# Kernel optimization log

Hardware: AMD Instinct MI355X
Metric: run time of the kernel (lower is better)

## Reference

```python
import jax, jax.numpy as jnp
import numpy as np

D_MODEL, NHEAD = 256, 8
HEAD_DIM = D_MODEL // NHEAD  # 32, also the conv group count


def layer_norm(x, w, b, eps=1e-5):
    mu = jnp.mean(x, axis=-1, keepdims=True)
    var = jnp.var(x, axis=-1, keepdims=True)
    return (x - mu) * jax.lax.rsqrt(var + eps) * w + b


def setup_inputs() -> dict:
    key = jax.random.key(0)
    ks = jax.random.split(key, 12)
    b, H, W = 4, 120, 160
    L = H * W  # 19200; 'self' path requires L == H*W
    d, h = D_MODEL, NHEAD
    s = 0.05
    p = lambda i, shape: jax.random.normal(ks[i], shape, jnp.float32) * s
    return {
        "x": jax.random.normal(ks[0], (b, L, d), jnp.float32),
        "source": jax.random.normal(ks[1], (b, L, d), jnp.float32),
        "Wq": p(2, (d, d)), "Wk": p(3, (d, d)), "Wv": p(4, (d, d)),
        "Wmerge": p(5, (d, d)),
        "Wmlp1": p(6, (2 * d, 2 * d)), "Wmlp2": p(7, (2 * d, d)),
        "ln1_w": jnp.ones((d,), jnp.float32), "ln1_b": jnp.zeros((d,), jnp.float32),
        "ln2_w": jnp.ones((d,), jnp.float32), "ln2_b": jnp.zeros((d,), jnp.float32),
        "Wdown": p(8, (2 * d, 64)), "Wup": p(9, (64, d)),
        "fc_w": p(10, (9, 3 * h)), "fc_b": jnp.zeros((9,), jnp.float32),
        "dep_w": p(11, (d, 9, 3, 3)),  # torch OIHW layout, groups=32 (O/g=8, I/g=9)
        "dep_b": jnp.zeros((d,), jnp.float32),
        "rate": jnp.full((1,), 0.5, jnp.float32),
        "H": H, "W": W,
    }


def reference(x, source, Wq, Wk, Wv, Wmerge, Wmlp1, Wmlp2,
              ln1_w, ln1_b, ln2_w, ln2_b, Wdown, Wup,
              fc_w, fc_b, dep_w, dep_b, rate, H, W):
    # name == 'self' path is hardcoded (conv branch active)
    b, L, d = x.shape
    h, hd = NHEAD, HEAD_DIM
    S = source.shape[1]

    q = (x @ Wq).reshape(b, L, h, hd)
    k = (source @ Wk).reshape(b, S, h, hd)
    v = (source @ Wv).reshape(b, S, h, hd)

    # ---- conv branch ----
    # [b, L, h, 3*hd] -> [b, L, 3h, hd] -> [b, 3h, L, hd]
    f_all = jnp.concatenate([q, k, v], axis=-1).reshape(b, L, 3 * h, hd)
    f_all = jnp.transpose(f_all, (0, 2, 1, 3))
    # 1x1 conv 3h -> 9 over (L, hd) 'spatial' grid
    f9 = jnp.einsum('oc,bcld->bold', fc_w, f_all) + fc_b[None, :, None, None]
    # [b, 9, L, hd] -> [b, hd, 9, L] -> [b, 9*hd, H, W]
    f_conv = jnp.transpose(f9, (0, 3, 1, 2)).reshape(b, 9 * hd, H, W)
    out_conv = jax.lax.conv_general_dilated(
        f_conv, dep_w, window_strides=(1, 1), padding=((1, 1), (1, 1)),
        feature_group_count=hd, dimension_numbers=('NCHW', 'OIHW', 'NCHW'))
    out_conv = out_conv + dep_b[None, :, None, None]
    out_conv = jnp.transpose(out_conv, (0, 2, 3, 1)).reshape(b, L, d)

    # ---- linear attention (elu+1 feature map), O(N) ----
    Qf = jax.nn.elu(q) + 1.0
    Kf = jax.nn.elu(k) + 1.0
    v_len = jnp.float32(S)
    vals = v / v_len
    KV = jnp.einsum('bshd,bshv->bhdv', Kf, vals)
    Z = 1.0 / (jnp.einsum('blhd,bhd->blh', Qf, Kf.sum(axis=1)) + 1e-6)
    message = jnp.einsum('blhd,bhdv,blh->blhv', Qf, KV, Z) * v_len

    # ---- merge / norm / MLP / adapter ----
    message = message.reshape(b, L, d) @ Wmerge
    message = layer_norm(message, ln1_w, ln1_b)
    cat1 = jnp.concatenate([x, message], axis=2)
    message = jax.nn.relu(cat1 @ Wmlp1) @ Wmlp2
    message = layer_norm(message, ln2_w, ln2_b)

    cat2 = jnp.concatenate([x, message], axis=2)
    up = jax.nn.relu(cat2 @ Wdown) @ Wup
    message = message + up * 0.1
    message = message + rate * out_conv
    return x + message
```

## Files before the change

kernel.cpp:

```cpp
#include <hip/hip_runtime.h>
#include <stdint.h>

#define LL 19200
#define NBATCH 4
#define NROWS (NBATCH * LL)
#define HH 120
#define WW 160

typedef short bhalf8 __attribute__((ext_vector_type(8)));
typedef float f32x4 __attribute__((ext_vector_type(4)));

__device__ __forceinline__ float bfbits2f(uint32_t u) { union { uint32_t i; float f; } c; c.i = u << 16; return c.f; }
__device__ __forceinline__ float bf2f(uint16_t h) { return bfbits2f((uint32_t)h); }
__device__ __forceinline__ uint16_t f2bf(float f) {
    union { float f; uint32_t i; } c; c.f = f;
    return (uint16_t)((c.i + 0x7FFFu + ((c.i >> 16) & 1u)) >> 16);
}
__device__ __forceinline__ uint32_t pk2(uint16_t a, uint16_t b) { return (uint32_t)a | ((uint32_t)b << 16); }
__device__ __forceinline__ float elup1(float x) { return x > 0.f ? x + 1.f : expf(x); }

__device__ __forceinline__ uint4 pack8f(const float* p) {
    float4 lo = *(const float4*)p; float4 hi = *(const float4*)(p + 4);
    uint4 s;
    s.x = pk2(f2bf(lo.x), f2bf(lo.y)); s.y = pk2(f2bf(lo.z), f2bf(lo.w));
    s.z = pk2(f2bf(hi.x), f2bf(hi.y)); s.w = pk2(f2bf(hi.z), f2bf(hi.w));
    return s;
}

__device__ __forceinline__ void gll16(const void* g, void* l) {
    __builtin_amdgcn_global_load_lds((const __attribute__((address_space(1))) uint32_t*)g,
                                     (__attribute__((address_space(3))) uint32_t*)l, 16, 0, 0);
}

__global__ __launch_bounds__(256) void prep_wt(const float* __restrict__ src, uint16_t* __restrict__ dst,
                                               int K, int Nout) {
    int idx = blockIdx.x * 256 + threadIdx.x;
    if (idx >= K * Nout) return;
    int n = idx / K, kk = idx - n * K;
    dst[idx] = f2bf(src[(long)kk * Nout + n]);
}

#define EPI_NONE 0
#define EPI_RELU 1
#define EPI_LN 2
#define EPI_FINAL 3

template<int BN, int MODE_A, int EPI>
__global__ __launch_bounds__(512)
void gemm_big(const float* __restrict__ A0f, const uint16_t* __restrict__ A0b,
              const uint16_t* __restrict__ A1b,
              const uint16_t* __restrict__ Wt, int K,
              uint16_t* __restrict__ outb, float* __restrict__ outf, int outW,
              const float* __restrict__ lnw, const float* __restrict__ lnb,
              const float* __restrict__ xres, const uint16_t* __restrict__ msg2res,
              const uint16_t* __restrict__ convres, const float* __restrict__ ratep)
{
    constexpr int WCOLS = BN / 64;
    constexpr int WROWS = 8 / WCOLS;
    constexpr int MT = 128 / (WROWS * 16);
    __shared__ __align__(16) uint16_t a_sm[128 * 32];
    __shared__ __align__(16) uint16_t b_sm[BN * 32];
    const int tid = threadIdx.x;
    const int lane = tid & 63;
    const int wv = tid >> 6;
    const int wr = wv / WCOLS, wc = wv % WCOLS;
    const long row0 = (long)blockIdx.x * 128;
    const int col0 = blockIdx.y * BN;

    f32x4 acc[MT][4];
#pragma unroll
    for (int m = 0; m < MT; ++m)
#pragma unroll
        for (int n = 0; n < 4; ++n) acc[m][n] = (f32x4){0.f, 0.f, 0.f, 0.f};

    const int sr = tid >> 2;
    const int sc = (tid & 3) * 8;
    const long argA = row0 + sr;
    uint16_t* a_dst = a_sm + (tid >> 6) * 512;
    uint16_t* b_dst = b_sm + (tid >> 6) * 512;

    for (int k0 = 0; k0 < K; k0 += 32) {
        if (MODE_A == 0) {
            gll16(A0b + argA * (long)K + k0 + sc, a_dst);
        } else if (MODE_A == 1) {
            *(uint4*)&a_sm[sr * 32 + sc] = pack8f(A0f + argA * (long)K + k0 + sc);
        } else {
            if (k0 < 256) *(uint4*)&a_sm[sr * 32 + sc] = pack8f(A0f + argA * 256 + k0 + sc);
            else          gll16(A1b + argA * 256 + (k0 - 256) + sc, a_dst);
        }
        if (BN == 256) {
            gll16(Wt + (long)(col0 + sr) * K + k0 + sc, b_dst);
            gll16(Wt + (long)(col0 + 128 + sr) * K + k0 + sc, b_sm + 4096 + (tid >> 6) * 512);
        } else {
            if (tid < 256) gll16(Wt + (long)(col0 + sr) * K + k0 + sc, b_dst);
        }
        __syncthreads();
        bhalf8 af[MT];
#pragma unroll
        for (int m = 0; m < MT; ++m)
            af[m] = *(const bhalf8*)&a_sm[(wr * MT * 16 + m * 16 + (lane & 15)) * 32 + (lane >> 4) * 8];
#pragma unroll
        for (int n = 0; n < 4; ++n) {
            bhalf8 bfr = *(const bhalf8*)&b_sm[(wc * 64 + n * 16 + (lane & 15)) * 32 + (lane >> 4) * 8];
#pragma unroll
            for (int m = 0; m < MT; ++m)
                acc[m][n] = __builtin_amdgcn_mfma_f32_16x16x32_bf16(af[m], bfr, acc[m][n], 0, 0, 0);
        }
        __syncthreads();
    }

    const int cl = lane & 15;
    const int rg4 = (lane >> 4) * 4;

    if constexpr (EPI == EPI_LN) {
        __shared__ float red_s[4][128];
        __shared__ float red_ss[4][128];
#pragma unroll
        for (int m = 0; m < MT; ++m)
#pragma unroll
            for (int j = 0; j < 4; ++j) {
                float p = 0.f, pp = 0.f;
#pragma unroll
                for (int n = 0; n < 4; ++n) { float v = acc[m][n][j]; p += v; pp += v * v; }
#pragma unroll
                for (int msk = 1; msk < 16; msk <<= 1) { p += __shfl_xor(p, msk, 64); pp += __shfl_xor(pp, msk, 64); }
                if (cl == 0) {
                    int lr = wr * 64 + m * 16 + rg4 + j;
                    red_s[wc][lr] = p; red_ss[wc][lr] = pp;
                }
            }
        __syncthreads();
#pragma unroll
        for (int m = 0; m < MT; ++m)
#pragma unroll
            for (int j = 0; j < 4; ++j) {
                int lr = wr * 64 + m * 16 + rg4 + j;
                float s = red_s[0][lr] + red_s[1][lr] + red_s[2][lr] + red_s[3][lr];
                float ss = red_ss[0][lr] + red_ss[1][lr] + red_ss[2][lr] + red_ss[3][lr];
                float mu = s * (1.f / 256.f);
                float var = ss * (1.f / 256.f) - mu * mu;
                float rstd = rsqrtf(var + 1e-5f);
                long rowg = row0 + lr;
#pragma unroll
                for (int n = 0; n < 4; ++n) {
                    int col = wc * 64 + n * 16 + cl;
                    float vv = (acc[m][n][j] - mu) * rstd * lnw[col] + lnb[col];
                    outb[rowg * (long)outW + col] = f2bf(vv);
                }
            }
    } else if constexpr (EPI == EPI_FINAL) {
        float rate = ratep[0];
#pragma unroll
        for (int m = 0; m < MT; ++m)
#pragma unroll
            for (int j = 0; j < 4; ++j) {
                long rowg = row0 + wr * MT * 16 + m * 16 + rg4 + j;
                int bb = (int)(rowg / LL);
                int ll = (int)(rowg - (long)bb * LL);
#pragma unroll
                for (int n = 0; n < 4; ++n) {
                    int col = wc * 64 + n * 16 + cl;
                    long o = rowg * 256 + col;
                    float xv = xres[o];
                    float m2 = bf2f(msg2res[o]);
                    float cv = bf2f(convres[((long)(bb * 256 + col)) * LL + ll]);
                    outf[o] = xv + m2 + 0.1f * acc[m][n][j] + rate * cv;
                }
            }
    } else {
#pragma unroll
        for (int m = 0; m < MT; ++m)
#pragma unroll
            for (int j = 0; j < 4; ++j) {
                long rowg = row0 + wr * MT * 16 + m * 16 + rg4 + j;
#pragma unroll
                for (int n = 0; n < 4; ++n) {
                    int col = col0 + wc * 64 + n * 16 + cl;
                    float vv = acc[m][n][j];
                    if (EPI == EPI_RELU) vv = vv > 0.f ? vv : 0.f;
                    outb[rowg * (long)outW + col] = f2bf(vv);
                }
            }
    }
}

__global__ __launch_bounds__(256)
void kv_partial(const uint16_t* __restrict__ kb, const uint16_t* __restrict__ vb,
                float* __restrict__ part) {
    __shared__ float kf_sm[32][33];
    __shared__ float v_sm[32][33];
    const int tid = threadIdx.x;
    const int bh = blockIdx.y, b = bh >> 3, h = bh & 7;
    const int s0 = blockIdx.x * 256;
    const int d = tid >> 3, vg = tid & 7;
    const int sl = tid >> 3, e4 = (tid & 7) * 4;
    float a0 = 0.f, a1 = 0.f, a2 = 0.f, a3 = 0.f, aKs = 0.f;
    for (int it = 0; it < 8; ++it) {
        long base = ((long)(b * LL + s0 + it * 32 + sl)) * 256 + h * 32 + e4;
        uint2 kk = *(const uint2*)(kb + base);
        uint2 vv = *(const uint2*)(vb + base);
        kf_sm[sl][e4 + 0] = elup1(bfbits2f(kk.x & 0xFFFFu));
        kf_sm[sl][e4 + 1] = elup1(bfbits2f(kk.x >> 16));
        kf_sm[sl][e4 + 2] = elup1(bfbits2f(kk.y & 0xFFFFu));
        kf_sm[sl][e4 + 3] = elup1(bfbits2f(kk.y >> 16));
        v_sm[sl][e4 + 0] = bfbits2f(vv.x & 0xFFFFu);
        v_sm[sl][e4 + 1] = bfbits2f(vv.x >> 16);
        v_sm[sl][e4 + 2] = bfbits2f(vv.y & 0xFFFFu);
        v_sm[sl][e4 + 3] = bfbits2f(vv.y >> 16);
        __syncthreads();
#pragma unroll 8
        for (int s = 0; s < 32; ++s) {
            float kf = kf_sm[s][d];
            aKs += kf;
            const float* vp = &v_sm[s][vg * 4];
            a0 += kf * vp[0]; a1 += kf * vp[1]; a2 += kf * vp[2]; a3 += kf * vp[3];
        }
        __syncthreads();
    }
    long pb = ((long)(blockIdx.x * 32 + bh)) * 1056;
    part[pb + d * 32 + vg * 4 + 0] = a0;
    part[pb + d * 32 + vg * 4 + 1] = a1;
    part[pb + d * 32 + vg * 4 + 2] = a2;
    part[pb + d * 32 + vg * 4 + 3] = a3;
    if (vg == 0) part[pb + 1024 + d] = aKs;
}

__global__ __launch_bounds__(256)
void kv_final(const float* __restrict__ part, float* __restrict__ KVg, float* __restrict__ Ksum) {
    const int bh = blockIdx.x, tid = threadIdx.x;
    for (int idx = tid; idx < 1056; idx += 256) {
        float s = 0.f;
        for (int c = 0; c < 75; ++c) s += part[((long)(c * 32 + bh)) * 1056 + idx];
        if (idx < 1024) KVg[bh * 1024 + idx] = s;
        else Ksum[bh * 32 + idx - 1024] = s;
    }
}

__global__ __launch_bounds__(256)
void attn_msg(const uint16_t* __restrict__ qb, const float* __restrict__ KVg,
              const float* __restrict__ Ksum, uint16_t* __restrict__ msgout) {
    __shared__ float kv_sm[8192];
    __shared__ float ks_sm[256];
    __shared__ float qf_sm[8][264];
    const int tid = threadIdx.x;
    const int b = blockIdx.y;
    const long l0 = (long)blockIdx.x * 64;
    for (int idx = tid; idx < 8192; idx += 256) kv_sm[idx] = KVg[b * 8192 + idx];
    ks_sm[tid] = Ksum[b * 256 + tid];
    __syncthreads();
    const int h = tid >> 5, vc = tid & 31;
    const int rr = tid >> 5, e8 = (tid & 31) * 8;
    for (int r0 = 0; r0 < 64; r0 += 8) {
        long rowg = (long)b * LL + l0 + r0 + rr;
        uint4 qv = *(const uint4*)(qb + rowg * 256 + e8);
        qf_sm[rr][e8 + 0] = elup1(bfbits2f(qv.x & 0xFFFFu));
        qf_sm[rr][e8 + 1] = elup1(bfbits2f(qv.x >> 16));
        qf_sm[rr][e8 + 2] = elup1(bfbits2f(qv.y & 0xFFFFu));
        qf_sm[rr][e8 + 3] = elup1(bfbits2f(qv.y >> 16));
        qf_sm[rr][e8 + 4] = elup1(bfbits2f(qv.z & 0xFFFFu));
        qf_sm[rr][e8 + 5] = elup1(bfbits2f(qv.z >> 16));
        qf_sm[rr][e8 + 6] = elup1(bfbits2f(qv.w & 0xFFFFu));
        qf_sm[rr][e8 + 7] = elup1(bfbits2f(qv.w >> 16));
        __syncthreads();
        for (int r2 = 0; r2 < 8; ++r2) {
            float p = qf_sm[r2][h * 32 + vc] * ks_sm[h * 32 + vc];
#pragma unroll
            for (int m = 1; m < 32; m <<= 1) p += __shfl_xor(p, m, 64);
            float Z = 1.f / (p + 1e-6f);
            float acc = 0.f;
#pragma unroll
            for (int dd = 0; dd < 32; ++dd)
                acc += qf_sm[r2][h * 32 + dd] * kv_sm[(h * 32 + dd) * 32 + vc];
            long orow = (long)b * LL + l0 + r0 + r2;
            msgout[orow * 256 + tid] = f2bf(acc * Z);
        }
        __syncthreads();
    }
}

__global__ __launch_bounds__(256)
void f9_kernel(const uint16_t* __restrict__ qb, const uint16_t* __restrict__ kb,
               const uint16_t* __restrict__ vb, const float* __restrict__ fcw,
               const float* __restrict__ fcb, uint16_t* __restrict__ fconv) {
    __shared__ __align__(16) uint16_t sm[3][32][264];
    __shared__ float fw[9][24];
    __shared__ float fb[9];
    const int tid = threadIdx.x;
    const int b = blockIdx.y;
    const int l0 = blockIdx.x * 32;
    if (tid < 216) fw[tid / 24][tid % 24] = fcw[tid];
    if (tid >= 216 && tid < 225) fb[tid - 216] = fcb[tid - 216];
    for (int idx = tid; idx < 3072; idx += 256) {
        int tsr = idx >> 10, rem = idx & 1023, row = rem >> 5, c8 = (rem & 31) * 8;
        const uint16_t* src = tsr == 0 ? qb : (tsr == 1 ? kb : vb);
        *(uint4*)&sm[tsr][row][c8] = *(const uint4*)(src + ((long)(b * LL + l0 + row)) * 256 + c8);
    }
    __syncthreads();
    for (int idx = tid; idx < 9216; idx += 256) {
        int ch = idx >> 5, li = idx & 31;
        int dp = ch / 9, o = ch - dp * 9;
        float acc = fb[o];
#pragma unroll
        for (int hd = 0; hd < 8; ++hd) {
            int cb = hd * 32 + dp;
            acc += fw[o][3 * hd + 0] * bf2f(sm[0][li][cb]);
            acc += fw[o][3 * hd + 1] * bf2f(sm[1][li][cb]);
            acc += fw[o][3 * hd + 2] * bf2f(sm[2][li][cb]);
        }
        fconv[((long)(b * 288 + ch)) * LL + l0 + li] = f2bf(acc);
    }
}

__global__ __launch_bounds__(256)
void dwconv2(const uint16_t* __restrict__ fconv, const float* __restrict__ depw,
             const float* __restrict__ depb, uint16_t* __restrict__ convout) {
    __shared__ __align__(16) uint16_t in_sm[9][26][48];
    __shared__ float w_sm[8][81];
    __shared__ float b_sm2[8];
    const int tid = threadIdx.x;
    const int bg = blockIdx.z, b = bg >> 5, g = bg & 31;
    const int y0 = blockIdx.y * 24;
    const int x0 = blockIdx.x * 32;
    for (int idx = tid; idx < 648; idx += 256)
        w_sm[idx / 81][idx % 81] = depw[(long)(g * 8) * 81 + idx];
    if (tid < 8) b_sm2[tid] = depb[g * 8 + tid];
    for (int rIdx = tid; rIdx < 234; rIdx += 256) {
        int i = rIdx / 26, r = rIdx - i * 26;
        int yy = y0 + r - 1;
        uint16_t* dst = &in_sm[i][r][0];
        if (yy >= 0 && yy < HH) {
            const uint16_t* rp = fconv + ((long)(b * 288 + g * 9 + i)) * LL + yy * WW;
            *(uint4*)&dst[8]  = *(const uint4*)(rp + x0);
            *(uint4*)&dst[16] = *(const uint4*)(rp + x0 + 8);
            *(uint4*)&dst[24] = *(const uint4*)(rp + x0 + 16);
            *(uint4*)&dst[32] = *(const uint4*)(rp + x0 + 24);
            dst[7]  = (x0 > 0) ? rp[x0 - 1] : (uint16_t)0;
            dst[40] = (x0 + 32 < WW) ? rp[x0 + 32] : (uint16_t)0;
        } else {
            uint4 z = {0, 0, 0, 0};
            *(uint4*)&dst[8] = z; *(uint4*)&dst[16] = z;
            *(uint4*)&dst[24] = z; *(uint4*)&dst[32] = z;
            dst[7] = 0; dst[40] = 0;
        }
    }
    __syncthreads();
    const int xc = tid & 7, m = (tid >> 3) & 7, ys = tid >> 6;
    float acc[6][4];
    float bias = b_sm2[m];
#pragma unroll
    for (int r = 0; r < 6; ++r)
#pragma unroll
        for (int o = 0; o < 4; ++o) acc[r][o] = bias;
    for (int i = 0; i < 9; ++i) {
        float w[9];
#pragma unroll
        for (int t = 0; t < 9; ++t) w[t] = w_sm[m][i * 9 + t];
#pragma unroll
        for (int rr = 0; rr < 8; ++rr) {
            const uint16_t* rowb = &in_sm[i][ys * 6 + rr][4 + xc * 4];
            uint2 lo = *(const uint2*)rowb;
            uint2 hi = *(const uint2*)(rowb + 4);
            uint32_t ex = *(const uint32_t*)(rowb + 8);
            float f[6];
            f[0] = bfbits2f(lo.y >> 16);
            f[1] = bfbits2f(hi.x & 0xFFFFu);
            f[2] = bfbits2f(hi.x >> 16);
            f[3] = bfbits2f(hi.y & 0xFFFFu);
            f[4] = bfbits2f(hi.y >> 16);
            f[5] = bfbits2f(ex & 0xFFFFu);
#pragma unroll
            for (int ky = 0; ky < 3; ++ky) {
                int ro = rr - ky;
                if (ro >= 0 && ro < 6) {
#pragma unroll
                    for (int o = 0; o < 4; ++o)
                        acc[ro][o] += w[ky * 3 + 0] * f[o] + w[ky * 3 + 1] * f[o + 1] + w[ky * 3 + 2] * f[o + 2];
                }
            }
        }
    }
    long chbase = ((long)(b * 256 + g * 8 + m)) * LL;
#pragma unroll
    for (int rl = 0; rl < 6; ++rl) {
        int y = y0 + ys * 6 + rl;
        uint2 st;
        st.x = pk2(f2bf(acc[rl][0]), f2bf(acc[rl][1]));
        st.y = pk2(f2bf(acc[rl][2]), f2bf(acc[rl][3]));
        *(uint2*)(convout + chbase + (long)y * WW + x0 + xc * 4) = st;
    }
}

extern "C" void kernel_launch(void* const* d_in, const int* in_sizes, int n_in,
                              void* d_out, int out_size, void* d_ws, size_t ws_size,
                              hipStream_t stream) {
    (void)in_sizes; (void)n_in; (void)out_size; (void)ws_size;
    const float* x      = (const float*)d_in[0];
    const float* src    = (const float*)d_in[1];
    const float* Wq     = (const float*)d_in[2];
    const float* Wk     = (const float*)d_in[3];
    const float* Wv     = (const float*)d_in[4];
    const float* Wmerge = (const float*)d_in[5];
    const float* Wmlp1  = (const float*)d_in[6];
    const float* Wmlp2  = (const float*)d_in[7];
    const float* ln1w   = (const float*)d_in[8];
    const float* ln1b   = (const float*)d_in[9];
    const float* ln2w   = (const float*)d_in[10];
    const float* ln2b   = (const float*)d_in[11];
    const float* Wdown  = (const float*)d_in[12];
    const float* Wup    = (const float*)d_in[13];
    const float* fcw    = (const float*)d_in[14];
    const float* fcb    = (const float*)d_in[15];
    const float* depw   = (const float*)d_in[16];
    const float* depb   = (const float*)d_in[17];
    const float* rate   = (const float*)d_in[18];

    char* ws = (char*)d_ws;
    const size_t SZ_NB = (size_t)NROWS * 256 * 2;
    const size_t O_Q = 0;
    const size_t O_K = SZ_NB;
    const size_t O_V = 2 * SZ_NB;
    const size_t O_FCONV = 3 * SZ_NB;
    const size_t O_CONVOUT = O_FCONV + (size_t)NBATCH * 288 * LL * 2;
    const size_t O_PART = O_CONVOUT + SZ_NB;
    const size_t O_KV = O_PART + (size_t)75 * 32 * 1056 * 4;
    const size_t O_KS = O_KV + (size_t)32 * 1024 * 4;
    const size_t O_WT = O_KS + (size_t)32 * 32 * 4;

    uint16_t* qB      = (uint16_t*)(ws + O_Q);
    uint16_t* kB      = (uint16_t*)(ws + O_K);
    uint16_t* vB      = (uint16_t*)(ws + O_V);
    uint16_t* fconv   = (uint16_t*)(ws + O_FCONV);
    uint16_t* convout = (uint16_t*)(ws + O_CONVOUT);
    float*    part    = (float*)(ws + O_PART);
    float*    KVg     = (float*)(ws + O_KV);
    float*    Ksg     = (float*)(ws + O_KS);
    uint16_t* wt_q    = (uint16_t*)(ws + O_WT);
    uint16_t* wt_k    = wt_q + 256 * 256;
    uint16_t* wt_v    = wt_k + 256 * 256;
    uint16_t* wt_m    = wt_v + 256 * 256;
    uint16_t* wt_m1   = wt_m + 256 * 256;
    uint16_t* wt_m2   = wt_m1 + 512 * 512;
    uint16_t* wt_d    = wt_m2 + 512 * 256;
    uint16_t* wt_u    = wt_d + 512 * 64;
    uint16_t* msgattn = kB;
    uint16_t* msgB    = vB;
    uint16_t* hidden  = qB;
    uint16_t* msg2    = fconv;
    uint16_t* h2      = (uint16_t*)(ws + O_PART);

    prep_wt<<<256, 256, 0, stream>>>(Wq, wt_q, 256, 256);
    prep_wt<<<256, 256, 0, stream>>>(Wk, wt_k, 256, 256);
    prep_wt<<<256, 256, 0, stream>>>(Wv, wt_v, 256, 256);
    prep_wt<<<256, 256, 0, stream>>>(Wmerge, wt_m, 256, 256);
    prep_wt<<<1024, 256, 0, stream>>>(Wmlp1, wt_m1, 512, 512);
    prep_wt<<<512, 256, 0, stream>>>(Wmlp2, wt_m2, 512, 256);
    prep_wt<<<128, 256, 0, stream>>>(Wdown, wt_d, 512, 64);
    prep_wt<<<64, 256, 0, stream>>>(Wup, wt_u, 64, 256);

    const dim3 g600(NROWS / 128, 1);
    gemm_big<256, 1, EPI_NONE><<<g600, 512, 0, stream>>>(x, nullptr, nullptr, wt_q, 256, qB, nullptr, 256,
        nullptr, nullptr, nullptr, nullptr, nullptr, nullptr);
    gemm_big<256, 1, EPI_NONE><<<g600, 512, 0, stream>>>(src, nullptr, nullptr, wt_k, 256, kB, nullptr, 256,
        nullptr, nullptr, nullptr, nullptr, nullptr, nullptr);
    gemm_big<256, 1, EPI_NONE><<<g600, 512, 0, stream>>>(src, nullptr, nullptr, wt_v, 256, vB, nullptr, 256,
        nullptr, nullptr, nullptr, nullptr, nullptr, nullptr);
    kv_partial<<<dim3(75, 32), 256, 0, stream>>>(kB, vB, part);
    kv_final<<<32, 256, 0, stream>>>(part, KVg, Ksg);
    f9_kernel<<<dim3(LL / 32, NBATCH), 256, 0, stream>>>(qB, kB, vB, fcw, fcb, fconv);
    dwconv2<<<dim3(5, 5, 128), 256, 0, stream>>>(fconv, depw, depb, convout);
    attn_msg<<<dim3(LL / 64, NBATCH), 256, 0, stream>>>(qB, KVg, Ksg, msgattn);
    gemm_big<256, 0, EPI_LN><<<g600, 512, 0, stream>>>(nullptr, msgattn, nullptr, wt_m, 256, msgB, nullptr, 256,
        ln1w, ln1b, nullptr, nullptr, nullptr, nullptr);
    gemm_big<256, 2, EPI_RELU><<<dim3(NROWS / 128, 2), 512, 0, stream>>>(x, nullptr, msgB, wt_m1, 512, hidden, nullptr, 512,
        nullptr, nullptr, nullptr, nullptr, nullptr, nullptr);
    gemm_big<256, 0, EPI_LN><<<g600, 512, 0, stream>>>(nullptr, hidden, nullptr, wt_m2, 512, msg2, nullptr, 256,
        ln2w, ln2b, nullptr, nullptr, nullptr, nullptr);
    gemm_big<64, 2, EPI_RELU><<<g600, 512, 0, stream>>>(x, nullptr, msg2, wt_d, 512, h2, nullptr, 64,
        nullptr, nullptr, nullptr, nullptr, nullptr, nullptr);
    gemm_big<256, 0, EPI_FINAL><<<g600, 512, 0, stream>>>(nullptr, h2, nullptr, wt_u, 64, nullptr, (float*)d_out, 256,
        nullptr, nullptr, x, msg2, convout, rate);
}
```

Baseline: 956.8 us.

## Cache bf16 copies of inputs, MFMA attention, swizzled f9, fused weight prep

Several independent changes land together. The Q and K projections now write bf16 copies of x and source as a side output, and later GEMMs (V, MLP1, down-projection and the final residual) read these instead of reloading and repacking fp32, which cuts input bandwidth. The attention-message kernel is rewritten around MFMA 16x16x32 bf16 tiles, f9_kernel is restructured with XOR-swizzled LDS and register accumulation, kv_partial uses float4 LDS accesses, and the eight weight-prep launches become one. Reading x as bf16 for the final residual adds rounding error to the output, and the bf16-copy path only runs when the workspace is large enough.

```diff
diff --git a/kernel.cpp b/kernel.cpp
--- a/kernel.cpp
+++ b/kernel.cpp
@@ -32,12 +32,29 @@
                                      (__attribute__((address_space(3))) uint32_t*)l, 16, 0, 0);
 }
 
-__global__ __launch_bounds__(256) void prep_wt(const float* __restrict__ src, uint16_t* __restrict__ dst,
-                                               int K, int Nout) {
-    int idx = blockIdx.x * 256 + threadIdx.x;
-    if (idx >= K * Nout) return;
+__global__ __launch_bounds__(256)
+void prep_all(const float* __restrict__ Wq, const float* __restrict__ Wk,
+              const float* __restrict__ Wv, const float* __restrict__ Wm,
+              const float* __restrict__ Wm1, const float* __restrict__ Wm2,
+              const float* __restrict__ Wd, const float* __restrict__ Wu,
+              uint16_t* __restrict__ wq, uint16_t* __restrict__ wk,
+              uint16_t* __restrict__ wvv, uint16_t* __restrict__ wm,
+              uint16_t* __restrict__ wm1, uint16_t* __restrict__ wm2,
+              uint16_t* __restrict__ wd, uint16_t* __restrict__ wu) {
+    int blk = blockIdx.x;
+    const float* s; uint16_t* d; int K, N, base;
+    if (blk < 1024) {
+        int which = blk >> 8; base = which << 8;
+        s = which == 0 ? Wq : which == 1 ? Wk : which == 2 ? Wv : Wm;
+        d = which == 0 ? wq : which == 1 ? wk : which == 2 ? wvv : wm;
+        K = 256; N = 256;
+    } else if (blk < 2048) { s = Wm1; d = wm1; K = 512; N = 512; base = 1024; }
+    else if (blk < 2560)   { s = Wm2; d = wm2; K = 512; N = 256; base = 2048; }
+    else if (blk < 2688)   { s = Wd;  d = wd;  K = 512; N = 64;  base = 2560; }
+    else                   { s = Wu;  d = wu;  K = 64;  N = 256; base = 2688; }
+    int idx = (blk - base) * 256 + threadIdx.x;
     int n = idx / K, kk = idx - n * K;
-    dst[idx] = f2bf(src[(long)kk * Nout + n]);
+    d[idx] = f2bf(s[(long)kk * N + n]);
 }
 
 #define EPI_NONE 0
@@ -51,8 +68,10 @@
               const uint16_t* __restrict__ A1b,
               const uint16_t* __restrict__ Wt, int K,
               uint16_t* __restrict__ outb, float* __restrict__ outf, int outW,
+              uint16_t* __restrict__ sideout,
               const float* __restrict__ lnw, const float* __restrict__ lnb,
-              const float* __restrict__ xres, const uint16_t* __restrict__ msg2res,
+              const float* __restrict__ xres, const uint16_t* __restrict__ xresb,
+              const uint16_t* __restrict__ msg2res,
               const uint16_t* __restrict__ convres, const float* __restrict__ ratep)
 {
     constexpr int WCOLS = BN / 64;
@@ -76,21 +95,27 @@
     const int sr = tid >> 2;
     const int sc = (tid & 3) * 8;
     const long argA = row0 + sr;
-    uint16_t* a_dst = a_sm + (tid >> 6) * 512;
-    uint16_t* b_dst = b_sm + (tid >> 6) * 512;
+    uint16_t* a_dst = a_sm + wv * 512;
+    uint16_t* b_dst = b_sm + wv * 512;
 
     for (int k0 = 0; k0 < K; k0 += 32) {
         if (MODE_A == 0) {
             gll16(A0b + argA * (long)K + k0 + sc, a_dst);
         } else if (MODE_A == 1) {
-            *(uint4*)&a_sm[sr * 32 + sc] = pack8f(A0f + argA * (long)K + k0 + sc);
-        } else {
+            uint4 stg = pack8f(A0f + argA * (long)K + k0 + sc);
+            *(uint4*)&a_sm[sr * 32 + sc] = stg;
+            if (sideout) *(uint4*)(sideout + argA * (long)K + k0 + sc) = stg;
+        } else if (MODE_A == 2) {
             if (k0 < 256) *(uint4*)&a_sm[sr * 32 + sc] = pack8f(A0f + argA * 256 + k0 + sc);
             else          gll16(A1b + argA * 256 + (k0 - 256) + sc, a_dst);
+        } else {
+            const uint16_t* srcp = (k0 < 256) ? (A0b + argA * 256 + k0 + sc)
+                                              : (A1b + argA * 256 + (k0 - 256) + sc);
+            gll16(srcp, a_dst);
         }
         if (BN == 256) {
             gll16(Wt + (long)(col0 + sr) * K + k0 + sc, b_dst);
-            gll16(Wt + (long)(col0 + 128 + sr) * K + k0 + sc, b_sm + 4096 + (tid >> 6) * 512);
+            gll16(Wt + (long)(col0 + 128 + sr) * K + k0 + sc, b_sm + 4096 + wv * 512);
         } else {
             if (tid < 256) gll16(Wt + (long)(col0 + sr) * K + k0 + sc, b_dst);
         }
@@ -161,7 +186,7 @@
                 for (int n = 0; n < 4; ++n) {
                     int col = wc * 64 + n * 16 + cl;
                     long o = rowg * 256 + col;
-                    float xv = xres[o];
+                    float xv = xresb ? bf2f(xresb[o]) : xres[o];
                     float m2 = bf2f(msg2res[o]);
                     float cv = bf2f(convres[((long)(bb * 256 + col)) * LL + ll]);
                     outf[o] = xv + m2 + 0.1f * acc[m][n][j] + rate * cv;
@@ -188,7 +213,7 @@
 void kv_partial(const uint16_t* __restrict__ kb, const uint16_t* __restrict__ vb,
                 float* __restrict__ part) {
     __shared__ float kf_sm[32][33];
-    __shared__ float v_sm[32][33];
+    __shared__ float v_sm[32][36];
     const int tid = threadIdx.x;
     const int bh = blockIdx.y, b = bh >> 3, h = bh & 7;
     const int s0 = blockIdx.x * 256;
@@ -203,17 +228,17 @@
         kf_sm[sl][e4 + 1] = elup1(bfbits2f(kk.x >> 16));
         kf_sm[sl][e4 + 2] = elup1(bfbits2f(kk.y & 0xFFFFu));
         kf_sm[sl][e4 + 3] = elup1(bfbits2f(kk.y >> 16));
-        v_sm[sl][e4 + 0] = bfbits2f(vv.x & 0xFFFFu);
-        v_sm[sl][e4 + 1] = bfbits2f(vv.x >> 16);
-        v_sm[sl][e4 + 2] = bfbits2f(vv.y & 0xFFFFu);
-        v_sm[sl][e4 + 3] = bfbits2f(vv.y >> 16);
+        float4 vf;
+        vf.x = bfbits2f(vv.x & 0xFFFFu); vf.y = bfbits2f(vv.x >> 16);
+        vf.z = bfbits2f(vv.y & 0xFFFFu); vf.w = bfbits2f(vv.y >> 16);
+        *(float4*)&v_sm[sl][e4] = vf;
         __syncthreads();
 #pragma unroll 8
         for (int s = 0; s < 32; ++s) {
             float kf = kf_sm[s][d];
             aKs += kf;
-            const float* vp = &v_sm[s][vg * 4];
-            a0 += kf * vp[0]; a1 += kf * vp[1]; a2 += kf * vp[2]; a3 += kf * vp[3];
+            float4 v4 = *(const float4*)&v_sm[s][vg * 4];
+            a0 += kf * v4.x; a1 += kf * v4.y; a2 += kf * v4.z; a3 += kf * v4.w;
         }
         __syncthreads();
     }
@@ -237,44 +262,57 @@
 }
 
 __global__ __launch_bounds__(256)
-void attn_msg(const uint16_t* __restrict__ qb, const float* __restrict__ KVg,
-              const float* __restrict__ Ksum, uint16_t* __restrict__ msgout) {
-    __shared__ float kv_sm[8192];
-    __shared__ float ks_sm[256];
-    __shared__ float qf_sm[8][264];
+void attn_mfma(const uint16_t* __restrict__ qb, const float* __restrict__ KVg,
+               const float* __restrict__ Ksum, uint16_t* __restrict__ msgout) {
     const int tid = threadIdx.x;
-    const int b = blockIdx.y;
+    const int lane = tid & 63;
+    const int wv = tid >> 6;
     const long l0 = (long)blockIdx.x * 64;
-    for (int idx = tid; idx < 8192; idx += 256) kv_sm[idx] = KVg[b * 8192 + idx];
-    ks_sm[tid] = Ksum[b * 256 + tid];
-    __syncthreads();
-    const int h = tid >> 5, vc = tid & 31;
-    const int rr = tid >> 5, e8 = (tid & 31) * 8;
-    for (int r0 = 0; r0 < 64; r0 += 8) {
-        long rowg = (long)b * LL + l0 + r0 + rr;
-        uint4 qv = *(const uint4*)(qb + rowg * 256 + e8);
-        qf_sm[rr][e8 + 0] = elup1(bfbits2f(qv.x & 0xFFFFu));
-        qf_sm[rr][e8 + 1] = elup1(bfbits2f(qv.x >> 16));
-        qf_sm[rr][e8 + 2] = elup1(bfbits2f(qv.y & 0xFFFFu));
-        qf_sm[rr][e8 + 3] = elup1(bfbits2f(qv.y >> 16));
-        qf_sm[rr][e8 + 4] = elup1(bfbits2f(qv.z & 0xFFFFu));
-        qf_sm[rr][e8 + 5] = elup1(bfbits2f(qv.z >> 16));
-        qf_sm[rr][e8 + 6] = elup1(bfbits2f(qv.w & 0xFFFFu));
-        qf_sm[rr][e8 + 7] = elup1(bfbits2f(qv.w >> 16));
-        __syncthreads();
-        for (int r2 = 0; r2 < 8; ++r2) {
-            float p = qf_sm[r2][h * 32 + vc] * ks_sm[h * 32 + vc];
-#pragma unroll
-            for (int m = 1; m < 32; m <<= 1) p += __shfl_xor(p, m, 64);
-            float Z = 1.f / (p + 1e-6f);
-            float acc = 0.f;
-#pragma unroll
-            for (int dd = 0; dd < 32; ++dd)
-                acc += qf_sm[r2][h * 32 + dd] * kv_sm[(h * 32 + dd) * 32 + vc];
-            long orow = (long)b * LL + l0 + r0 + r2;
-            msgout[orow * 256 + tid] = f2bf(acc * Z);
-        }
-        __syncthreads();
+    const int b = (int)(l0 / LL);
+    const int l15 = lane & 15, lk = lane >> 4;
+#pragma unroll
+    for (int hi = 0; hi < 2; ++hi) {
+        const int h = wv * 2 + hi;
+        const float* kvb = KVg + ((long)(b * 8 + h)) * 1024;
+        const float* ksb = Ksum + (b * 8 + h) * 32;
+        bhalf8 B0, B1;
+        float ks[8];
+#pragma unroll
+        for (int i = 0; i < 8; ++i) {
+            int k = lk * 8 + i;
+            B0[i] = (short)f2bf(kvb[k * 32 + l15]);
+            B1[i] = (short)f2bf(kvb[k * 32 + 16 + l15]);
+            ks[i] = ksb[k];
+        }
+#pragma unroll
+        for (int rt = 0; rt < 4; ++rt) {
+            long row = l0 + rt * 16 + l15;
+            uint4 qv = *(const uint4*)(qb + row * 256 + h * 32 + lk * 8);
+            float qf[8];
+            qf[0] = elup1(bfbits2f(qv.x & 0xFFFFu)); qf[1] = elup1(bfbits2f(qv.x >> 16));
+            qf[2] = elup1(bfbits2f(qv.y & 0xFFFFu)); qf[3] = elup1(bfbits2f(qv.y >> 16));
+            qf[4] = elup1(bfbits2f(qv.z & 0xFFFFu)); qf[5] = elup1(bfbits2f(qv.z >> 16));
+            qf[6] = elup1(bfbits2f(qv.w & 0xFFFFu)); qf[7] = elup1(bfbits2f(qv.w >> 16));
+            bhalf8 A;
+#pragma unroll
+            for (int i = 0; i < 8; ++i) A[i] = (short)f2bf(qf[i]);
+            float p = qf[0]*ks[0] + qf[1]*ks[1] + qf[2]*ks[2] + qf[3]*ks[3]
+                    + qf[4]*ks[4] + qf[5]*ks[5] + qf[6]*ks[6] + qf[7]*ks[7];
+            p += __shfl_xor(p, 16, 64);
+            p += __shfl_xor(p, 32, 64);
+            f32x4 d0 = (f32x4){0.f,0.f,0.f,0.f}, d1 = (f32x4){0.f,0.f,0.f,0.f};
+            d0 = __builtin_amdgcn_mfma_f32_16x16x32_bf16(A, B0, d0, 0, 0, 0);
+            d1 = __builtin_amdgcn_mfma_f32_16x16x32_bf16(A, B1, d1, 0, 0, 0);
+#pragma unroll
+            for (int j = 0; j < 4; ++j) {
+                int orl = lk * 4 + j;
+                float zr = __shfl(p, orl, 64);
+                float Z = 1.f / (zr + 1e-6f);
+                long orow = l0 + rt * 16 + orl;
+                msgout[orow * 256 + h * 32 + l15]      = f2bf(d0[j] * Z);
+                msgout[orow * 256 + h * 32 + 16 + l15] = f2bf(d1[j] * Z);
+            }
+        }
     }
 }
 
@@ -282,32 +320,55 @@
 void f9_kernel(const uint16_t* __restrict__ qb, const uint16_t* __restrict__ kb,
                const uint16_t* __restrict__ vb, const float* __restrict__ fcw,
                const float* __restrict__ fcb, uint16_t* __restrict__ fconv) {
-    __shared__ __align__(16) uint16_t sm[3][32][264];
-    __shared__ float fw[9][24];
-    __shared__ float fb[9];
+    __shared__ __align__(16) uint16_t sm[3 * 32 * 256];
+    char* smb = (char*)sm;
     const int tid = threadIdx.x;
     const int b = blockIdx.y;
     const int l0 = blockIdx.x * 32;
-    if (tid < 216) fw[tid / 24][tid % 24] = fcw[tid];
-    if (tid >= 216 && tid < 225) fb[tid - 216] = fcb[tid - 216];
     for (int idx = tid; idx < 3072; idx += 256) {
-        int tsr = idx >> 10, rem = idx & 1023, row = rem >> 5, c8 = (rem & 31) * 8;
+        int tsr = idx >> 10, row = (idx >> 5) & 31, c = idx & 31;
         const uint16_t* src = tsr == 0 ? qb : (tsr == 1 ? kb : vb);
-        *(uint4*)&sm[tsr][row][c8] = *(const uint4*)(src + ((long)(b * LL + l0 + row)) * 256 + c8);
+        uint4 v = *(const uint4*)(src + ((long)(b * LL + l0 + row)) * 256 + c * 8);
+        int boff = (c * 16) ^ ((row & 7) << 4);
+        *(uint4*)(smb + (tsr * 32 + row) * 512 + boff) = v;
     }
     __syncthreads();
-    for (int idx = tid; idx < 9216; idx += 256) {
-        int ch = idx >> 5, li = idx & 31;
-        int dp = ch / 9, o = ch - dp * 9;
-        float acc = fb[o];
-#pragma unroll
-        for (int hd = 0; hd < 8; ++hd) {
-            int cb = hd * 32 + dp;
-            acc += fw[o][3 * hd + 0] * bf2f(sm[0][li][cb]);
-            acc += fw[o][3 * hd + 1] * bf2f(sm[1][li][cb]);
-            acc += fw[o][3 * hd + 2] * bf2f(sm[2][li][cb]);
-        }
-        fconv[((long)(b * 288 + ch)) * LL + l0 + li] = f2bf(acc);
+    const int li = tid & 31, g = tid >> 5;
+    float acc[9][4];
+#pragma unroll
+    for (int o = 0; o < 9; ++o) {
+        float bv = fcb[o];
+#pragma unroll
+        for (int j = 0; j < 4; ++j) acc[o][j] = bv;
+    }
+    const int swz = (li & 7) << 4;
+#pragma unroll
+    for (int h = 0; h < 8; ++h) {
+        float f[3][4];
+#pragma unroll
+        for (int s = 0; s < 3; ++s) {
+            int boff = (h * 64 + g * 8) ^ swz;
+            uint2 r = *(const uint2*)(smb + (s * 32 + li) * 512 + boff);
+            f[s][0] = bfbits2f(r.x & 0xFFFFu); f[s][1] = bfbits2f(r.x >> 16);
+            f[s][2] = bfbits2f(r.y & 0xFFFFu); f[s][3] = bfbits2f(r.y >> 16);
+        }
+#pragma unroll
+        for (int o = 0; o < 9; ++o) {
+            float w0 = fcw[o * 24 + 3 * h + 0];
+            float w1 = fcw[o * 24 + 3 * h + 1];
+            float w2 = fcw[o * 24 + 3 * h + 2];
+#pragma unroll
+            for (int j = 0; j < 4; ++j)
+                acc[o][j] += w0 * f[0][j] + w1 * f[1][j] + w2 * f[2][j];
+        }
+    }
+    const long ob = (long)(b * 288) * LL + l0 + li;
+#pragma unroll
+    for (int j = 0; j < 4; ++j) {
+        int dp = g * 4 + j;
+#pragma unroll
+        for (int o = 0; o < 9; ++o)
+            fconv[ob + (long)(dp * 9 + o) * LL] = f2bf(acc[o][j]);
     }
 }
 
@@ -344,7 +405,7 @@
         }
     }
     __syncthreads();
-    const int xc = tid & 7, m = (tid >> 3) & 7, ys = tid >> 6;
+    const int xi = tid & 7, m = (tid >> 3) & 7, ys = tid >> 6;
     float acc[6][4];
     float bias = b_sm2[m];
 #pragma unroll
@@ -357,7 +418,7 @@
         for (int t = 0; t < 9; ++t) w[t] = w_sm[m][i * 9 + t];
 #pragma unroll
         for (int rr = 0; rr < 8; ++rr) {
-            const uint16_t* rowb = &in_sm[i][ys * 6 + rr][4 + xc * 4];
+            const uint16_t* rowb = &in_sm[i][ys * 6 + rr][4 + xi * 4];
             uint2 lo = *(const uint2*)rowb;
             uint2 hi = *(const uint2*)(rowb + 4);
             uint32_t ex = *(const uint32_t*)(rowb + 8);
@@ -386,14 +447,14 @@
         uint2 st;
         st.x = pk2(f2bf(acc[rl][0]), f2bf(acc[rl][1]));
         st.y = pk2(f2bf(acc[rl][2]), f2bf(acc[rl][3]));
-        *(uint2*)(convout + chbase + (long)y * WW + x0 + xc * 4) = st;
+        *(uint2*)(convout + chbase + (long)y * WW + x0 + xi * 4) = st;
     }
 }
 
 extern "C" void kernel_launch(void* const* d_in, const int* in_sizes, int n_in,
                               void* d_out, int out_size, void* d_ws, size_t ws_size,
                               hipStream_t stream) {
-    (void)in_sizes; (void)n_in; (void)out_size; (void)ws_size;
+    (void)in_sizes; (void)n_in; (void)out_size;
     const float* x      = (const float*)d_in[0];
     const float* src    = (const float*)d_in[1];
     const float* Wq     = (const float*)d_in[2];
@@ -425,6 +486,9 @@
     const size_t O_KV = O_PART + (size_t)75 * 32 * 1056 * 4;
     const size_t O_KS = O_KV + (size_t)32 * 1024 * 4;
     const size_t O_WT = O_KS + (size_t)32 * 32 * 4;
+    const size_t O_XB = O_WT + 704512 * 2 + 1024;
+    const size_t O_SRCB = O_XB + SZ_NB;
+    const size_t NEED = O_SRCB + SZ_NB;
 
     uint16_t* qB      = (uint16_t*)(ws + O_Q);
     uint16_t* kB      = (uint16_t*)(ws + O_K);
@@ -442,41 +506,54 @@
     uint16_t* wt_m2   = wt_m1 + 512 * 512;
     uint16_t* wt_d    = wt_m2 + 512 * 256;
     uint16_t* wt_u    = wt_d + 512 * 64;
+    uint16_t* xb      = (uint16_t*)(ws + O_XB);
+    uint16_t* srcb    = (uint16_t*)(ws + O_SRCB);
     uint16_t* msgattn = kB;
     uint16_t* msgB    = vB;
     uint16_t* hidden  = qB;
     uint16_t* msg2    = fconv;
     uint16_t* h2      = (uint16_t*)(ws + O_PART);
 
-    prep_wt<<<256, 256, 0, stream>>>(Wq, wt_q, 256, 256);
-    prep_wt<<<256, 256, 0, stream>>>(Wk, wt_k, 256, 256);
-    prep_wt<<<256, 256, 0, stream>>>(Wv, wt_v, 256, 256);
-    prep_wt<<<256, 256, 0, stream>>>(Wmerge, wt_m, 256, 256);
-    prep_wt<<<1024, 256, 0, stream>>>(Wmlp1, wt_m1, 512, 512);
-    prep_wt<<<512, 256, 0, stream>>>(Wmlp2, wt_m2, 512, 256);
-    prep_wt<<<128, 256, 0, stream>>>(Wdown, wt_d, 512, 64);
-    prep_wt<<<64, 256, 0, stream>>>(Wup, wt_u, 64, 256);
+    const bool big = ws_size >= NEED;
+
+    prep_all<<<2752, 256, 0, stream>>>(Wq, Wk, Wv, Wmerge, Wmlp1, Wmlp2, Wdown, Wup,
+                                       wt_q, wt_k, wt_v, wt_m, wt_m1, wt_m2, wt_d, wt_u);
 
     const dim3 g600(NROWS / 128, 1);
     gemm_big<256, 1, EPI_NONE><<<g600, 512, 0, stream>>>(x, nullptr, nullptr, wt_q, 256, qB, nullptr, 256,
-        nullptr, nullptr, nullptr, nullptr, nullptr, nullptr);
+        big ? xb : nullptr, nullptr, nullptr, nullptr, nullptr, nullptr, nullptr, nullptr);
     gemm_big<256, 1, EPI_NONE><<<g600, 512, 0, stream>>>(src, nullptr, nullptr, wt_k, 256, kB, nullptr, 256,
-        nullptr, nullptr, nullptr, nullptr, nullptr, nullptr);
-    gemm_big<256, 1, EPI_NONE><<<g600, 512, 0, stream>>>(src, nullptr, nullptr, wt_v, 256, vB, nullptr, 256,
-        nullptr, nullptr, nullptr, nullptr, nullptr, nullptr);
+        big ? srcb : nullptr, nullptr, nullptr, nullptr, nullptr, nullptr, nullptr, nullptr);
+    if (big) {
+        gemm_big<256, 0, EPI_NONE><<<g600, 512, 0, stream>>>(nullptr, srcb, nullptr, wt_v, 256, vB, nullptr, 256,
+            nullptr, nullptr, nullptr, nullptr, nullptr, nullptr, nullptr, nullptr);
+    } else {
+        gemm_big<256, 1, EPI_NONE><<<g600, 512, 0, stream>>>(src, nullptr, nullptr, wt_v, 256, vB, nullptr, 256,
+            nullptr, nullptr, nullptr, nullptr, nullptr, nullptr, nullptr, nullptr);
+    }
     kv_partial<<<dim3(75, 32), 256, 0, stream>>>(kB, vB, part);
     kv_final<<<32, 256, 0, stream>>>(part, KVg, Ksg);
     f9_kernel<<<dim3(LL / 32, NBATCH), 256, 0, stream>>>(qB, kB, vB, fcw, fcb, fconv);
     dwconv2<<<dim3(5, 5, 128), 256, 0, stream>>>(fconv, depw, depb, convout);
-    attn_msg<<<dim3(LL / 64, NBATCH), 256, 0, stream>>>(qB, KVg, Ksg, msgattn);
+    attn_mfma<<<NROWS / 64, 256, 0, stream>>>(qB, KVg, Ksg, msgattn);
     gemm_big<256, 0, EPI_LN><<<g600, 512, 0, stream>>>(nullptr, msgattn, nullptr, wt_m, 256, msgB, nullptr, 256,
-        ln1w, ln1b, nullptr, nullptr, nullptr, nullptr);
-    gemm_big<256, 2, EPI_RELU><<<dim3(NROWS / 128, 2), 512, 0, stream>>>(x, nullptr, msgB, wt_m1, 512, hidden, nullptr, 512,
-        nullptr, nullptr, nullptr, nullptr, nullptr, nullptr);
+        nullptr, ln1w, ln1b, nullptr, nullptr, nullptr, nullptr, nullptr);
+    if (big) {
+        gemm_big<256, 3, EPI_RELU><<<dim3(NROWS / 128, 2), 512, 0, stream>>>(nullptr, xb, msgB, wt_m1, 512, hidden, nullptr, 512,
+            nullptr, nullptr, nullptr, nullptr, nullptr, nullptr, nullptr, nullptr);
+    } else {
+        gemm_big<256, 2, EPI_RELU><<<dim3(NROWS / 128, 2), 512, 0, stream>>>(x, nullptr, msgB, wt_m1, 512, hidden, nullptr, 512,
+            nullptr, nullptr, nullptr, nullptr, nullptr, nullptr, nullptr, nullptr);
+    }
     gemm_big<256, 0, EPI_LN><<<g600, 512, 0, stream>>>(nullptr, hidden, nullptr, wt_m2, 512, msg2, nullptr, 256,
-        ln2w, ln2b, nullptr, nullptr, nullptr, nullptr);
-    gemm_big<64, 2, EPI_RELU><<<g600, 512, 0, stream>>>(x, nullptr, msg2, wt_d, 512, h2, nullptr, 64,
-        nullptr, nullptr, nullptr, nullptr, nullptr, nullptr);
+        nullptr, ln2w, ln2b, nullptr, nullptr, nullptr, nullptr, nullptr);
+    if (big) {
+        gemm_big<64, 3, EPI_RELU><<<g600, 512, 0, stream>>>(nullptr, xb, msg2, wt_d, 512, h2, nullptr, 64,
+            nullptr, nullptr, nullptr, nullptr, nullptr, nullptr, nullptr, nullptr);
+    } else {
+        gemm_big<64, 2, EPI_RELU><<<g600, 512, 0, stream>>>(x, nullptr, msg2, wt_d, 512, h2, nullptr, 64,
+            nullptr, nullptr, nullptr, nullptr, nullptr, nullptr, nullptr, nullptr);
+    }
     gemm_big<256, 0, EPI_FINAL><<<g600, 512, 0, stream>>>(nullptr, h2, nullptr, wt_u, 64, nullptr, (float*)d_out, 256,
-        nullptr, nullptr, x, msg2, convout, rate);
-}
+        nullptr, nullptr, nullptr, x, big ? xb : nullptr, msg2, convout, rate);
+}
```

Result: faster. 835.3 us (-12.7%).
